# Kernel tuning notes

Hardware: AMD Instinct MI355X
Metric: run time of the kernel (lower is better)

Reference implementation:

```python
import jax, jax.numpy as jnp
import numpy as np

EPS = 0.05
ITERS = 3
NORM_EPS = 1e-12  # torch F.normalize clamp


def setup_inputs() -> dict:
    key = jax.random.key(0)
    k1, k2, k3, k4 = jax.random.split(key, 4)
    x = jax.random.normal(k1, (16, 768, 64, 64), jnp.float32)
    conv_w = jax.random.normal(k2, (256, 768), jnp.float32) * 0.02  # 1x1 conv kernel [out,in]
    conv_b = jax.random.normal(k3, (256,), jnp.float32) * 0.02
    v = jax.random.normal(k4, (32, 256), jnp.float32)  # [num_clusters, token_dim]
    return {"x": x, "conv_w": conv_w, "conv_b": conv_b, "v": v}


def _l2_normalize(a, axis=-1):
    n = jnp.sqrt(jnp.sum(a * a, axis=axis, keepdims=True))
    return a / jnp.maximum(n, NORM_EPS)


def _log_optimal_transport(scores):
    # scores: [b, m, n]; log-domain Sinkhorn with uniform marginals
    b, m, n = scores.shape
    norm = -jnp.log(jnp.float32(m + n))
    Z = scores / EPS
    u = jnp.full((b, m), 0.0, Z.dtype)
    v = jnp.full((b, n), 0.0, Z.dtype)
    for _ in range(ITERS):
        u = norm - jax.scipy.special.logsumexp(Z + v[:, None, :], axis=2)
        v = norm - jax.scipy.special.logsumexp(Z + u[:, :, None], axis=1)
    return jnp.exp(Z + u[:, :, None] + v[:, None, :] - norm)


def reference(x, conv_w, conv_b, v):
    # 1x1 conv projection: [b, C, H, W] -> [b, D, H, W]
    xp = jnp.einsum('bchw,dc->bdhw', x, conv_w) + conv_b[None, :, None, None]
    b, d, H, W = xp.shape
    x_proj = xp.reshape(b, d, H * W).transpose(0, 2, 1)  # [b, hw, d]
    xf = _l2_normalize(x_proj)  # l2_normalize branch
    w = _l2_normalize(v)        # cluster weights normalized (in-place copy in torch)
    scores = jnp.einsum('bnd,md->bnm', xf, w)  # [b, hw, m]
    weights = _log_optimal_transport(scores.transpose(0, 2, 1)).transpose(0, 2, 1)  # [b, hw, m]
    v_tilde = jnp.einsum('bnd,bnm->bmd', xf, weights)  # [b, m, d]
    return (v_tilde, x_proj)
```

## Files before the change

### kernel.cpp

```cpp
#include <hip/hip_runtime.h>
#include <math.h>

#define NORM_C (-8.3255483f)

typedef __attribute__((ext_vector_type(8))) short bf16x8;
typedef __attribute__((ext_vector_type(4))) float f32x4;

union U8 { uint4 q; unsigned u[4]; bf16x8 v; };

__device__ inline unsigned short f2bf_rne(float f) {
    unsigned u = __float_as_uint(f);
    unsigned r = u + 0x7fffu + ((u >> 16) & 1u);
    return (unsigned short)(r >> 16);
}
__device__ inline unsigned pack_bf2(float lo, float hi) {
    unsigned a = __float_as_uint(lo) + 0x8000u;
    unsigned b = __float_as_uint(hi) + 0x8000u;
    return __builtin_amdgcn_perm(b, a, 0x07060302u);
}

__global__ __launch_bounds__(256) void w_cvt(const float* __restrict__ W,
                                             unsigned short* __restrict__ Wb) {
    int i = (blockIdx.x * 256 + threadIdx.x) * 4;
    float4 w = *(const float4*)(W + i);
    unsigned lo = (unsigned)f2bf_rne(w.x) | ((unsigned)f2bf_rne(w.y) << 16);
    unsigned hi = (unsigned)f2bf_rne(w.z) | ((unsigned)f2bf_rne(w.w) << 16);
    *(uint2*)(Wb + i) = make_uint2(lo, hi);
}

__global__ __launch_bounds__(64) void w_norm(const float* __restrict__ v_in,
                                             unsigned short* __restrict__ wnb) {
    const int lane = threadIdx.x;
    const int row = blockIdx.x;
    float4 v = *(const float4*)(v_in + row * 256 + lane * 4);
    float s = v.x * v.x + v.y * v.y + v.z * v.z + v.w * v.w;
#pragma unroll
    for (int off = 32; off > 0; off >>= 1) s += __shfl_xor(s, off);
    float inv = 1.0f / fmaxf(sqrtf(s), 1e-12f);
    unsigned lo = (unsigned)f2bf_rne(v.x * inv) | ((unsigned)f2bf_rne(v.y * inv) << 16);
    unsigned hi = (unsigned)f2bf_rne(v.z * inv) | ((unsigned)f2bf_rne(v.w * inv) << 16);
    *(uint2*)(wnb + row * 256 + lane * 4) = make_uint2(lo, hi);
}

__global__ __launch_bounds__(256) void conv_mfma(const float* __restrict__ x,
                                                 const unsigned short* __restrict__ Wb,
                                                 const float* __restrict__ bias,
                                                 float* __restrict__ xp,
                                                 float* __restrict__ inv_norm) {
    __shared__ unsigned As[256 * 20];
    __shared__ unsigned Bs[128 * 17];
    __shared__ float ssq_s[128];

    const int tid = threadIdx.x;
    const int lane = tid & 63;
    const int wid = tid >> 6;
    const int wn = wid & 1, wd = wid >> 1;
    const int b = blockIdx.y;
    const int n0 = blockIdx.x * 128;
    const int l15 = lane & 15, l4 = lane >> 4;
    const float* xb = x + (size_t)b * 768 * 4096;

    f32x4 acc[8][4];
#pragma unroll
    for (int i = 0; i < 8; ++i)
#pragma unroll
        for (int j = 0; j < 4; ++j) acc[i][j] = (f32x4){0.f, 0.f, 0.f, 0.f};

    for (int k0 = 0; k0 < 768; k0 += 32) {
        __syncthreads();
#pragma unroll
        for (int i = 0; i < 4; ++i) {
            int f = tid + i * 256;
            int dd = f >> 2, c8 = f & 3;
            uint4 w = *(const uint4*)(Wb + (size_t)dd * 768 + k0 + c8 * 8);
            *(uint4*)&As[dd * 20 + c8 * 4] = w;
        }
#pragma unroll
        for (int i = 0; i < 4; ++i) {
            int f = tid + i * 256;
            int n2 = f & 63, ch = f >> 6;
            const float* p = xb + (size_t)(k0 + 2 * ch) * 4096 + n0 + 2 * n2;
            float2 g0 = *(const float2*)p;
            float2 g1 = *(const float2*)(p + 4096);
            Bs[(2 * n2) * 17 + ch] = pack_bf2(g0.x, g1.x);
            Bs[(2 * n2 + 1) * 17 + ch] = pack_bf2(g0.y, g1.y);
        }
        __syncthreads();

        U8 af[8];
#pragma unroll
        for (int dt = 0; dt < 8; ++dt) {
            int row = wd * 128 + dt * 16 + l15;
            af[dt].q = *(uint4*)&As[row * 20 + l4 * 4];
        }
#pragma unroll
        for (int nt = 0; nt < 4; ++nt) {
            int col = wn * 64 + nt * 16 + l15;
            int base = col * 17 + l4 * 4;
            U8 bf;
            bf.u[0] = Bs[base]; bf.u[1] = Bs[base + 1];
            bf.u[2] = Bs[base + 2]; bf.u[3] = Bs[base + 3];
#pragma unroll
            for (int dt = 0; dt < 8; ++dt)
                acc[dt][nt] = __builtin_amdgcn_mfma_f32_16x16x32_bf16(
                    af[dt].v, bf.v, acc[dt][nt], 0, 0, 0);
        }
    }

    float ssq[4] = {0.f, 0.f, 0.f, 0.f};
#pragma unroll
    for (int dt = 0; dt < 8; ++dt) {
        int d = wd * 128 + dt * 16 + l4 * 4;
        float4 bi = *(const float4*)(bias + d);
#pragma unroll
        for (int nt = 0; nt < 4; ++nt) {
            int n = n0 + wn * 64 + nt * 16 + l15;
            float4 o = make_float4(acc[dt][nt].x + bi.x, acc[dt][nt].y + bi.y,
                                   acc[dt][nt].z + bi.z, acc[dt][nt].w + bi.w);
            *(float4*)(xp + ((size_t)(b * 4096 + n)) * 256 + d) = o;
            ssq[nt] += o.x * o.x + o.y * o.y + o.z * o.z + o.w * o.w;
        }
    }
#pragma unroll
    for (int nt = 0; nt < 4; ++nt) {
        ssq[nt] += __shfl_xor(ssq[nt], 16);
        ssq[nt] += __shfl_xor(ssq[nt], 32);
    }
    if (wd == 0 && l4 == 0) {
#pragma unroll
        for (int nt = 0; nt < 4; ++nt) ssq_s[wn * 64 + nt * 16 + l15] = ssq[nt];
    }
    __syncthreads();
    if (wd == 1 && l4 == 0) {
#pragma unroll
        for (int nt = 0; nt < 4; ++nt) {
            int nl = wn * 64 + nt * 16 + l15;
            float tot = ssq[nt] + ssq_s[nl];
            inv_norm[b * 4096 + n0 + nl] = 1.0f / fmaxf(sqrtf(tot), 1e-12f);
        }
    }
}

__global__ __launch_bounds__(256) void scores_mfma(const float* __restrict__ xp,
                                                   const float* __restrict__ inv_norm,
                                                   const unsigned short* __restrict__ wnb,
                                                   float* __restrict__ Z) {
    const int tid = threadIdx.x;
    const int lane = tid & 63;
    const int wid = tid >> 6;
    const int l15 = lane & 15, l4 = lane >> 4;
    const int b = blockIdx.y, ng = blockIdx.x;
    const int n = ng * 64 + wid * 16 + l15;

    U8 wf[2][8];
#pragma unroll
    for (int mt = 0; mt < 2; ++mt)
#pragma unroll
        for (int s = 0; s < 8; ++s)
            wf[mt][s].q = *(const uint4*)(wnb + (mt * 16 + l15) * 256 + s * 32 + l4 * 8);

    const float invs = inv_norm[b * 4096 + n] * 20.0f;
    const float* xr = xp + ((size_t)(b * 4096 + n)) * 256 + l4 * 8;

    f32x4 acc0 = {0.f, 0.f, 0.f, 0.f}, acc1 = {0.f, 0.f, 0.f, 0.f};
#pragma unroll
    for (int s = 0; s < 8; ++s) {
        float4 p0 = *(const float4*)(xr + s * 32);
        float4 p1 = *(const float4*)(xr + s * 32 + 4);
        U8 af;
        af.u[0] = pack_bf2(p0.x * invs, p0.y * invs);
        af.u[1] = pack_bf2(p0.z * invs, p0.w * invs);
        af.u[2] = pack_bf2(p1.x * invs, p1.y * invs);
        af.u[3] = pack_bf2(p1.z * invs, p1.w * invs);
        acc0 = __builtin_amdgcn_mfma_f32_16x16x32_bf16(af.v, wf[0][s].v, acc0, 0, 0, 0);
        acc1 = __builtin_amdgcn_mfma_f32_16x16x32_bf16(af.v, wf[1][s].v, acc1, 0, 0, 0);
    }
    const int n_out = ng * 64 + wid * 16 + l4 * 4;
    *(f32x4*)&Z[((size_t)(b * 32 + l15)) * 4096 + n_out] = acc0;
    *(f32x4*)&Z[((size_t)(b * 32 + 16 + l15)) * 4096 + n_out] = acc1;
}

template <int USE_V>
__global__ __launch_bounds__(256) void sink_u(const float* __restrict__ Z,
                                              const float* __restrict__ v_g,
                                              float* __restrict__ u_g) {
    __shared__ float wmx[4], wsum[4];
    const int tid = threadIdx.x;
    const int lane = tid & 63, wid = tid >> 6;
    const int b = blockIdx.x >> 5, m = blockIdx.x & 31;
    const float* zr = Z + ((size_t)(b * 32 + m)) * 4096;
    const float* vr = v_g + b * 4096;

    float z[16];
#pragma unroll
    for (int j = 0; j < 16; ++j) {
        int n = tid + j * 256;
        z[j] = USE_V ? (zr[n] + vr[n]) : zr[n];
    }
    float mx = z[0];
#pragma unroll
    for (int j = 1; j < 16; ++j) mx = fmaxf(mx, z[j]);
    float s = 0.f;
#pragma unroll
    for (int j = 0; j < 16; ++j) s += __expf(z[j] - mx);
#pragma unroll
    for (int off = 1; off < 64; off <<= 1) {
        float omx = __shfl_xor(mx, off);
        float os = __shfl_xor(s, off);
        float nm = fmaxf(mx, omx);
        s = s * __expf(mx - nm) + os * __expf(omx - nm);
        mx = nm;
    }
    if (lane == 0) { wmx[wid] = mx; wsum[wid] = s; }
    __syncthreads();
    if (tid == 0) {
        float gm = wmx[0], gs = wsum[0];
#pragma unroll
        for (int w = 1; w < 4; ++w) {
            float nm = fmaxf(gm, wmx[w]);
            gs = gs * __expf(gm - nm) + wsum[w] * __expf(wmx[w] - nm);
            gm = nm;
        }
        u_g[b * 32 + m] = NORM_C - (gm + __logf(gs));
    }
}

__global__ __launch_bounds__(512) void sink_v(const float* __restrict__ Z,
                                              const float* __restrict__ u_g,
                                              float* __restrict__ v_g) {
    __shared__ float u_s[32];
    const int tid = threadIdx.x;
    const int b = blockIdx.y;
    const int n = blockIdx.x * 512 + tid;
    if (tid < 32) u_s[tid] = u_g[b * 32 + tid];
    __syncthreads();
    float z[32];
#pragma unroll
    for (int m = 0; m < 32; ++m) z[m] = Z[((size_t)(b * 32 + m)) * 4096 + n] + u_s[m];
    float mx = z[0];
#pragma unroll
    for (int m = 1; m < 32; ++m) mx = fmaxf(mx, z[m]);
    float s = 0.f;
#pragma unroll
    for (int m = 0; m < 32; ++m) s += __expf(z[m] - mx);
    v_g[b * 4096 + n] = NORM_C - (mx + __logf(s));
}

__global__ __launch_bounds__(256) void vtilde_part_k(const float* __restrict__ xp,
                                                     const float* __restrict__ inv_norm,
                                                     const float* __restrict__ Z,
                                                     const float* __restrict__ u_g,
                                                     float* __restrict__ part) {
    __shared__ float u_s[32];
    __shared__ float v3_s[256];
    __shared__ float inv_s[256];
    __shared__ float wt[64 * 36];
    const int tid = threadIdx.x;
    const int cx = blockIdx.x;
    const int chunk = cx >> 1, dh = cx & 1;
    const int b = blockIdx.y;
    const int n0 = chunk * 256;
    if (tid < 32) u_s[tid] = u_g[b * 32 + tid];
    __syncthreads();
    {
        int n = n0 + tid;
        float z[32];
#pragma unroll
        for (int m = 0; m < 32; ++m)
            z[m] = Z[((size_t)(b * 32 + m)) * 4096 + n] + u_s[m];
        float mx = z[0];
#pragma unroll
        for (int m = 1; m < 32; ++m) mx = fmaxf(mx, z[m]);
        float s = 0.f;
#pragma unroll
        for (int m = 0; m < 32; ++m) s += __expf(z[m] - mx);
        v3_s[tid] = NORM_C - (mx + __logf(s));
        inv_s[tid] = inv_norm[b * 4096 + n];
    }
    __syncthreads();

    const int dg = tid & 31, mq = tid >> 5;
    f32x4 acc[4];
#pragma unroll
    for (int j = 0; j < 4; ++j) acc[j] = (f32x4){0.f, 0.f, 0.f, 0.f};
    const float* xpb = xp + ((size_t)(b * 4096 + n0)) * 256 + dh * 128 + dg * 4;

    for (int t = 0; t < 4; ++t) {
#pragma unroll
        for (int i = 0; i < 8; ++i) {
            int e = tid + i * 256;
            int mW = e >> 6, nn = e & 63;
            int nl = t * 64 + nn;
            wt[nn * 36 + mW] =
                __expf(Z[((size_t)(b * 32 + mW)) * 4096 + n0 + nl] + u_s[mW] +
                       v3_s[nl] - NORM_C) * inv_s[nl];
        }
        __syncthreads();
#pragma unroll 4
        for (int nn = 0; nn < 64; ++nn) {
            float4 xv = *(const float4*)(xpb + (size_t)(t * 64 + nn) * 256);
            float4 wv = *(const float4*)&wt[nn * 36 + mq * 4];
            acc[0].x += wv.x * xv.x; acc[0].y += wv.x * xv.y; acc[0].z += wv.x * xv.z; acc[0].w += wv.x * xv.w;
            acc[1].x += wv.y * xv.x; acc[1].y += wv.y * xv.y; acc[1].z += wv.y * xv.z; acc[1].w += wv.y * xv.w;
            acc[2].x += wv.z * xv.x; acc[2].y += wv.z * xv.y; acc[2].z += wv.z * xv.z; acc[2].w += wv.z * xv.w;
            acc[3].x += wv.w * xv.x; acc[3].y += wv.w * xv.y; acc[3].z += wv.w * xv.z; acc[3].w += wv.w * xv.w;
        }
        __syncthreads();
    }
#pragma unroll
    for (int j = 0; j < 4; ++j) {
        int m = mq * 4 + j;
        *(f32x4*)&part[((size_t)(b * 16 + chunk)) * 8192 + m * 256 + dh * 128 + dg * 4] = acc[j];
    }
}

__global__ __launch_bounds__(256) void vtilde_reduce(const float* __restrict__ part,
                                                     float* __restrict__ out_vt) {
    int o = blockIdx.x * 256 + threadIdx.x;
    int b = o >> 13, r = o & 8191;
    float s = 0.f;
#pragma unroll
    for (int c = 0; c < 16; ++c)
        s += part[((size_t)(b * 16 + c)) * 8192 + r];
    out_vt[o] = s;
}

extern "C" void kernel_launch(void* const* d_in, const int* in_sizes, int n_in,
                              void* d_out, int out_size, void* d_ws, size_t ws_size,
                              hipStream_t stream) {
    const float* x      = (const float*)d_in[0];
    const float* conv_w = (const float*)d_in[1];
    const float* conv_b = (const float*)d_in[2];
    const float* v_in   = (const float*)d_in[3];

    float* out_vt = (float*)d_out;
    float* out_xp = (float*)d_out + 131072;

    float* ws = (float*)d_ws;
    float*          inv_norm = ws;
    unsigned short* Wb       = (unsigned short*)(ws + 65536);
    unsigned short* wnb      = (unsigned short*)(ws + 163840);
    float*          Zbuf     = ws + 167936;
    float*          u_g      = ws + 2265088;
    float*          v_g      = ws + 2265600;
    float*          part     = ws + 2331136;

    w_cvt<<<192, 256, 0, stream>>>(conv_w, Wb);
    w_norm<<<32, 64, 0, stream>>>(v_in, wnb);
    conv_mfma<<<dim3(32, 16), 256, 0, stream>>>(x, Wb, conv_b, out_xp, inv_norm);
    scores_mfma<<<dim3(64, 16), 256, 0, stream>>>(out_xp, inv_norm, wnb, Zbuf);
    sink_u<0><<<512, 256, 0, stream>>>(Zbuf, v_g, u_g);
    sink_v<<<dim3(8, 16), 512, 0, stream>>>(Zbuf, u_g, v_g);
    sink_u<1><<<512, 256, 0, stream>>>(Zbuf, v_g, u_g);
    sink_v<<<dim3(8, 16), 512, 0, stream>>>(Zbuf, u_g, v_g);
    sink_u<1><<<512, 256, 0, stream>>>(Zbuf, v_g, u_g);
    vtilde_part_k<<<dim3(32, 16), 256, 0, stream>>>(out_xp, inv_norm, Zbuf, u_g, part);
    vtilde_reduce<<<512, 256, 0, stream>>>(part, out_vt);
}
```

Measured before the change: 382.5 us.

## Fuse scores GEMM and first Sinkhorn u-step into conv epilogue

The conv kernel's epilogue now normalizes the projected tile from registers, stages it in shared memory as bf16, and computes the cluster scores with MFMA. This removes the separate scores kernel and its re-read of the fp32 projection. Each block also emits partial max/sum logsumexp pairs for the first u update, which the first sink_v combines, so the first sink_u launch goes away. The two weight-prep kernels are merged into one launch. The cost is more LDS per block, which may lower conv occupancy, and extra serial work at the end of the conv kernel.

```diff
diff --git a/kernel.cpp b/kernel.cpp
--- a/kernel.cpp
+++ b/kernel.cpp
@@ -19,37 +19,44 @@
     return __builtin_amdgcn_perm(b, a, 0x07060302u);
 }
 
-__global__ __launch_bounds__(256) void w_cvt(const float* __restrict__ W,
-                                             unsigned short* __restrict__ Wb) {
-    int i = (blockIdx.x * 256 + threadIdx.x) * 4;
-    float4 w = *(const float4*)(W + i);
-    unsigned lo = (unsigned)f2bf_rne(w.x) | ((unsigned)f2bf_rne(w.y) << 16);
-    unsigned hi = (unsigned)f2bf_rne(w.z) | ((unsigned)f2bf_rne(w.w) << 16);
-    *(uint2*)(Wb + i) = make_uint2(lo, hi);
-}
-
-__global__ __launch_bounds__(64) void w_norm(const float* __restrict__ v_in,
+__global__ __launch_bounds__(64) void w_prep(const float* __restrict__ W,
+                                             const float* __restrict__ v_in,
+                                             unsigned short* __restrict__ Wb,
                                              unsigned short* __restrict__ wnb) {
-    const int lane = threadIdx.x;
-    const int row = blockIdx.x;
-    float4 v = *(const float4*)(v_in + row * 256 + lane * 4);
-    float s = v.x * v.x + v.y * v.y + v.z * v.z + v.w * v.w;
-#pragma unroll
-    for (int off = 32; off > 0; off >>= 1) s += __shfl_xor(s, off);
-    float inv = 1.0f / fmaxf(sqrtf(s), 1e-12f);
-    unsigned lo = (unsigned)f2bf_rne(v.x * inv) | ((unsigned)f2bf_rne(v.y * inv) << 16);
-    unsigned hi = (unsigned)f2bf_rne(v.z * inv) | ((unsigned)f2bf_rne(v.w * inv) << 16);
-    *(uint2*)(wnb + row * 256 + lane * 4) = make_uint2(lo, hi);
-}
-
-__global__ __launch_bounds__(256) void conv_mfma(const float* __restrict__ x,
+    const int bx = blockIdx.x, tid = threadIdx.x;
+    if (bx < 768) {
+        int i = (bx * 64 + tid) * 4;
+        float4 w = *(const float4*)(W + i);
+        unsigned lo = (unsigned)f2bf_rne(w.x) | ((unsigned)f2bf_rne(w.y) << 16);
+        unsigned hi = (unsigned)f2bf_rne(w.z) | ((unsigned)f2bf_rne(w.w) << 16);
+        *(uint2*)(Wb + i) = make_uint2(lo, hi);
+    } else {
+        int row = bx - 768;
+        float4 v = *(const float4*)(v_in + row * 256 + tid * 4);
+        float s = v.x * v.x + v.y * v.y + v.z * v.z + v.w * v.w;
+#pragma unroll
+        for (int off = 32; off > 0; off >>= 1) s += __shfl_xor(s, off);
+        float inv = 1.0f / fmaxf(sqrtf(s), 1e-12f);
+        unsigned lo = (unsigned)f2bf_rne(v.x * inv) | ((unsigned)f2bf_rne(v.y * inv) << 16);
+        unsigned hi = (unsigned)f2bf_rne(v.z * inv) | ((unsigned)f2bf_rne(v.w * inv) << 16);
+        *(uint2*)(wnb + row * 256 + tid * 4) = make_uint2(lo, hi);
+    }
+}
+
+__global__ __launch_bounds__(256) void conv_mega(const float* __restrict__ x,
                                                  const unsigned short* __restrict__ Wb,
                                                  const float* __restrict__ bias,
+                                                 const unsigned short* __restrict__ wnb,
                                                  float* __restrict__ xp,
-                                                 float* __restrict__ inv_norm) {
+                                                 float* __restrict__ inv_norm,
+                                                 float* __restrict__ Z,
+                                                 float2* __restrict__ u1p) {
     __shared__ unsigned As[256 * 20];
     __shared__ unsigned Bs[128 * 17];
     __shared__ float ssq_s[128];
+    __shared__ float invs_s[128];
+    __shared__ unsigned xfs[128 * 33];
+    __shared__ float2 upart_s[4][32];
 
     const int tid = threadIdx.x;
     const int lane = tid & 63;
@@ -115,9 +122,10 @@
 #pragma unroll
         for (int nt = 0; nt < 4; ++nt) {
             int n = n0 + wn * 64 + nt * 16 + l15;
-            float4 o = make_float4(acc[dt][nt].x + bi.x, acc[dt][nt].y + bi.y,
-                                   acc[dt][nt].z + bi.z, acc[dt][nt].w + bi.w);
-            *(float4*)(xp + ((size_t)(b * 4096 + n)) * 256 + d) = o;
+            f32x4 o = acc[dt][nt];
+            o.x += bi.x; o.y += bi.y; o.z += bi.z; o.w += bi.w;
+            acc[dt][nt] = o;
+            *(f32x4*)(xp + ((size_t)(b * 4096 + n)) * 256 + d) = o;
             ssq[nt] += o.x * o.x + o.y * o.y + o.z * o.z + o.w * o.w;
         }
     }
@@ -135,52 +143,141 @@
 #pragma unroll
         for (int nt = 0; nt < 4; ++nt) {
             int nl = wn * 64 + nt * 16 + l15;
-            float tot = ssq[nt] + ssq_s[nl];
-            inv_norm[b * 4096 + n0 + nl] = 1.0f / fmaxf(sqrtf(tot), 1e-12f);
-        }
-    }
-}
-
-__global__ __launch_bounds__(256) void scores_mfma(const float* __restrict__ xp,
-                                                   const float* __restrict__ inv_norm,
-                                                   const unsigned short* __restrict__ wnb,
-                                                   float* __restrict__ Z) {
+            float inv = 1.0f / fmaxf(sqrtf(ssq[nt] + ssq_s[nl]), 1e-12f);
+            invs_s[nl] = inv;
+            inv_norm[b * 4096 + n0 + nl] = inv;
+        }
+    }
+
+    f32x4 accz[2][2];
+#pragma unroll
+    for (int i = 0; i < 2; ++i)
+#pragma unroll
+        for (int j = 0; j < 2; ++j) accz[i][j] = (f32x4){0.f, 0.f, 0.f, 0.f};
+
+    for (int q = 0; q < 4; ++q) {
+        __syncthreads();
+        if (wd == (q >> 1)) {
+#pragma unroll
+            for (int dt4 = 0; dt4 < 4; ++dt4) {
+                int dt = (q & 1) * 4 + dt4;
+#pragma unroll
+                for (int nt = 0; nt < 4; ++nt) {
+                    int n = wn * 64 + nt * 16 + l15;
+                    float inv = invs_s[n];
+                    f32x4 a = acc[dt][nt];
+                    int base = n * 33 + dt4 * 8 + l4 * 2;
+                    xfs[base]     = pack_bf2(a.x * inv, a.y * inv);
+                    xfs[base + 1] = pack_bf2(a.z * inv, a.w * inv);
+                }
+            }
+        }
+        __syncthreads();
+#pragma unroll
+        for (int s = 0; s < 2; ++s) {
+            U8 wf[2];
+#pragma unroll
+            for (int mt = 0; mt < 2; ++mt)
+                wf[mt].q = *(const uint4*)(wnb + (mt * 16 + l15) * 256 +
+                                           q * 64 + s * 32 + l4 * 8);
+#pragma unroll
+            for (int sti = 0; sti < 2; ++sti) {
+                int st = wid + sti * 4;
+                int arow = (st * 16 + l15) * 33 + s * 16 + l4 * 4;
+                U8 af;
+                af.u[0] = xfs[arow]; af.u[1] = xfs[arow + 1];
+                af.u[2] = xfs[arow + 2]; af.u[3] = xfs[arow + 3];
+#pragma unroll
+                for (int mt = 0; mt < 2; ++mt)
+                    accz[sti][mt] = __builtin_amdgcn_mfma_f32_16x16x32_bf16(
+                        af.v, wf[mt].v, accz[sti][mt], 0, 0, 0);
+            }
+        }
+    }
+#pragma unroll
+    for (int sti = 0; sti < 2; ++sti)
+#pragma unroll
+        for (int mt = 0; mt < 2; ++mt) {
+            accz[sti][mt].x *= 20.f; accz[sti][mt].y *= 20.f;
+            accz[sti][mt].z *= 20.f; accz[sti][mt].w *= 20.f;
+            int m = mt * 16 + l15;
+            int st = wid + sti * 4;
+            *(f32x4*)&Z[((size_t)(b * 32 + m)) * 4096 + n0 + st * 16 + l4 * 4] =
+                accz[sti][mt];
+        }
+#pragma unroll
+    for (int mt = 0; mt < 2; ++mt) {
+        float v0[8] = {accz[0][mt].x, accz[0][mt].y, accz[0][mt].z, accz[0][mt].w,
+                       accz[1][mt].x, accz[1][mt].y, accz[1][mt].z, accz[1][mt].w};
+        float mx = v0[0];
+#pragma unroll
+        for (int i = 1; i < 8; ++i) mx = fmaxf(mx, v0[i]);
+        float s = 0.f;
+#pragma unroll
+        for (int i = 0; i < 8; ++i) s += __expf(v0[i] - mx);
+#pragma unroll
+        for (int off = 16; off < 64; off <<= 1) {
+            float omx = __shfl_xor(mx, off);
+            float os = __shfl_xor(s, off);
+            float nm = fmaxf(mx, omx);
+            s = s * __expf(mx - nm) + os * __expf(omx - nm);
+            mx = nm;
+        }
+        if (lane < 16) upart_s[wid][mt * 16 + lane] = make_float2(mx, s);
+    }
+    __syncthreads();
+    if (wid == 0 && lane < 32) {
+        float2 p = upart_s[0][lane];
+        float mx = p.x, s = p.y;
+#pragma unroll
+        for (int w = 1; w < 4; ++w) {
+            float2 qq = upart_s[w][lane];
+            float nm = fmaxf(mx, qq.x);
+            s = s * __expf(mx - nm) + qq.y * __expf(qq.x - nm);
+            mx = nm;
+        }
+        u1p[((size_t)b * 32 + blockIdx.x) * 32 + lane] = make_float2(mx, s);
+    }
+}
+
+template <int FIRST>
+__global__ __launch_bounds__(512) void sink_v(const float* __restrict__ Z,
+                                              const float2* __restrict__ u1p,
+                                              const float* __restrict__ u_g,
+                                              float* __restrict__ v_g) {
+    __shared__ float u_s[32];
     const int tid = threadIdx.x;
-    const int lane = tid & 63;
-    const int wid = tid >> 6;
-    const int l15 = lane & 15, l4 = lane >> 4;
-    const int b = blockIdx.y, ng = blockIdx.x;
-    const int n = ng * 64 + wid * 16 + l15;
-
-    U8 wf[2][8];
-#pragma unroll
-    for (int mt = 0; mt < 2; ++mt)
-#pragma unroll
-        for (int s = 0; s < 8; ++s)
-            wf[mt][s].q = *(const uint4*)(wnb + (mt * 16 + l15) * 256 + s * 32 + l4 * 8);
-
-    const float invs = inv_norm[b * 4096 + n] * 20.0f;
-    const float* xr = xp + ((size_t)(b * 4096 + n)) * 256 + l4 * 8;
-
-    f32x4 acc0 = {0.f, 0.f, 0.f, 0.f}, acc1 = {0.f, 0.f, 0.f, 0.f};
-#pragma unroll
-    for (int s = 0; s < 8; ++s) {
-        float4 p0 = *(const float4*)(xr + s * 32);
-        float4 p1 = *(const float4*)(xr + s * 32 + 4);
-        U8 af;
-        af.u[0] = pack_bf2(p0.x * invs, p0.y * invs);
-        af.u[1] = pack_bf2(p0.z * invs, p0.w * invs);
-        af.u[2] = pack_bf2(p1.x * invs, p1.y * invs);
-        af.u[3] = pack_bf2(p1.z * invs, p1.w * invs);
-        acc0 = __builtin_amdgcn_mfma_f32_16x16x32_bf16(af.v, wf[0][s].v, acc0, 0, 0, 0);
-        acc1 = __builtin_amdgcn_mfma_f32_16x16x32_bf16(af.v, wf[1][s].v, acc1, 0, 0, 0);
-    }
-    const int n_out = ng * 64 + wid * 16 + l4 * 4;
-    *(f32x4*)&Z[((size_t)(b * 32 + l15)) * 4096 + n_out] = acc0;
-    *(f32x4*)&Z[((size_t)(b * 32 + 16 + l15)) * 4096 + n_out] = acc1;
-}
-
-template <int USE_V>
+    const int b = blockIdx.y;
+    const int n = blockIdx.x * 512 + tid;
+    if (tid < 32) {
+        if (FIRST) {
+            float2 p = u1p[((size_t)b * 32) * 32 + tid];
+            float mx = p.x, s = p.y;
+#pragma unroll 4
+            for (int t = 1; t < 32; ++t) {
+                float2 q = u1p[((size_t)b * 32 + t) * 32 + tid];
+                float nm = fmaxf(mx, q.x);
+                s = s * __expf(mx - nm) + q.y * __expf(q.x - nm);
+                mx = nm;
+            }
+            u_s[tid] = NORM_C - (mx + __logf(s));
+        } else {
+            u_s[tid] = u_g[b * 32 + tid];
+        }
+    }
+    __syncthreads();
+    float z[32];
+#pragma unroll
+    for (int m = 0; m < 32; ++m) z[m] = Z[((size_t)(b * 32 + m)) * 4096 + n] + u_s[m];
+    float mx = z[0];
+#pragma unroll
+    for (int m = 1; m < 32; ++m) mx = fmaxf(mx, z[m]);
+    float s = 0.f;
+#pragma unroll
+    for (int m = 0; m < 32; ++m) s += __expf(z[m] - mx);
+    v_g[b * 4096 + n] = NORM_C - (mx + __logf(s));
+}
+
 __global__ __launch_bounds__(256) void sink_u(const float* __restrict__ Z,
                                               const float* __restrict__ v_g,
                                               float* __restrict__ u_g) {
@@ -195,7 +292,7 @@
 #pragma unroll
     for (int j = 0; j < 16; ++j) {
         int n = tid + j * 256;
-        z[j] = USE_V ? (zr[n] + vr[n]) : zr[n];
+        z[j] = zr[n] + vr[n];
     }
     float mx = z[0];
 #pragma unroll
@@ -223,27 +320,6 @@
         }
         u_g[b * 32 + m] = NORM_C - (gm + __logf(gs));
     }
-}
-
-__global__ __launch_bounds__(512) void sink_v(const float* __restrict__ Z,
-                                              const float* __restrict__ u_g,
-                                              float* __restrict__ v_g) {
-    __shared__ float u_s[32];
-    const int tid = threadIdx.x;
-    const int b = blockIdx.y;
-    const int n = blockIdx.x * 512 + tid;
-    if (tid < 32) u_s[tid] = u_g[b * 32 + tid];
-    __syncthreads();
-    float z[32];
-#pragma unroll
-    for (int m = 0; m < 32; ++m) z[m] = Z[((size_t)(b * 32 + m)) * 4096 + n] + u_s[m];
-    float mx = z[0];
-#pragma unroll
-    for (int m = 1; m < 32; ++m) mx = fmaxf(mx, z[m]);
-    float s = 0.f;
-#pragma unroll
-    for (int m = 0; m < 32; ++m) s += __expf(z[m] - mx);
-    v_g[b * 4096 + n] = NORM_C - (mx + __logf(s));
 }
 
 __global__ __launch_bounds__(256) void vtilde_part_k(const float* __restrict__ xp,
@@ -341,19 +417,18 @@
     unsigned short* Wb       = (unsigned short*)(ws + 65536);
     unsigned short* wnb      = (unsigned short*)(ws + 163840);
     float*          Zbuf     = ws + 167936;
-    float*          u_g      = ws + 2265088;
-    float*          v_g      = ws + 2265600;
-    float*          part     = ws + 2331136;
-
-    w_cvt<<<192, 256, 0, stream>>>(conv_w, Wb);
-    w_norm<<<32, 64, 0, stream>>>(v_in, wnb);
-    conv_mfma<<<dim3(32, 16), 256, 0, stream>>>(x, Wb, conv_b, out_xp, inv_norm);
-    scores_mfma<<<dim3(64, 16), 256, 0, stream>>>(out_xp, inv_norm, wnb, Zbuf);
-    sink_u<0><<<512, 256, 0, stream>>>(Zbuf, v_g, u_g);
-    sink_v<<<dim3(8, 16), 512, 0, stream>>>(Zbuf, u_g, v_g);
-    sink_u<1><<<512, 256, 0, stream>>>(Zbuf, v_g, u_g);
-    sink_v<<<dim3(8, 16), 512, 0, stream>>>(Zbuf, u_g, v_g);
-    sink_u<1><<<512, 256, 0, stream>>>(Zbuf, v_g, u_g);
+    float2*         u1p      = (float2*)(ws + 2265088);
+    float*          u_g      = ws + 2297856;
+    float*          v_g      = ws + 2298368;
+    float*          part     = ws + 2363904;
+
+    w_prep<<<800, 64, 0, stream>>>(conv_w, v_in, Wb, wnb);
+    conv_mega<<<dim3(32, 16), 256, 0, stream>>>(x, Wb, conv_b, wnb, out_xp,
+                                                inv_norm, Zbuf, u1p);
+    sink_v<1><<<dim3(8, 16), 512, 0, stream>>>(Zbuf, u1p, u_g, v_g);
+    sink_u<<<512, 256, 0, stream>>>(Zbuf, v_g, u_g);
+    sink_v<0><<<dim3(8, 16), 512, 0, stream>>>(Zbuf, u1p, u_g, v_g);
+    sink_u<<<512, 256, 0, stream>>>(Zbuf, v_g, u_g);
     vtilde_part_k<<<dim3(32, 16), 256, 0, stream>>>(out_xp, inv_norm, Zbuf, u_g, part);
     vtilde_reduce<<<512, 256, 0, stream>>>(part, out_vt);
 }
```

Measured after the change: 374.8 us. -2.0%, faster.
